# Optimization experiments

Hardware: AMD Instinct MI355X
Metric: run time of the kernel (lower is better)

## Reference

```python
import jax, jax.numpy as jnp
import numpy as np

THRESHOLD = 0.05
TOP_N = 300
NMS_THR = 0.6
POST_TOP_N = 100
MIN_SIZE = 0
N_CLASS = 81
C = N_CLASS - 1
STRIDES = (8, 16, 32, 64, 128)
IMG_H, IMG_W = 800, 1024
B = 16


def _level_hw(s):
    return (-(-IMG_H // s), -(-IMG_W // s))


def setup_inputs() -> dict:
    key = jax.random.key(0)
    inp = {}
    for li, s in enumerate(STRIDES):
        H, W = _level_hw(s)
        key, k1, k2, k3 = jax.random.split(key, 4)
        xs = (jnp.arange(W, dtype=jnp.float32) + 0.5) * s
        ys = (jnp.arange(H, dtype=jnp.float32) + 0.5) * s
        gx, gy = jnp.meshgrid(xs, ys)  # [H, W], row-major h*W+w flatten order
        inp[f"location{li}"] = jnp.stack([gx.reshape(-1), gy.reshape(-1)], -1)
        inp[f"cls{li}"] = jax.random.normal(k1, (B, C, H, W), jnp.float32)
        inp[f"box{li}"] = jax.random.uniform(k2, (B, 4, H, W), jnp.float32) * (4.0 * s)
        inp[f"ctr{li}"] = jax.random.normal(k3, (B, 1, H, W), jnp.float32)
    inp["img_h"] = IMG_H
    inp["img_w"] = IMG_W
    return inp


def _process_level(loc, cls, box, ctr, img_h, img_w):
    b, c, h, w = cls.shape
    cls = jax.nn.sigmoid(cls.transpose(0, 2, 3, 1).reshape(b, h * w, c))
    box = box.transpose(0, 2, 3, 1).reshape(b, h * w, 4)
    ctr = jax.nn.sigmoid(ctr.reshape(b, h * w))
    score = cls * ctr[:, :, None]                 # [B, HW, C]
    masked = jnp.where(cls > THRESHOLD, score, -1.0).reshape(b, -1)
    k = min(TOP_N, masked.shape[1])
    vals, idx = jax.lax.top_k(masked, k)
    if k < TOP_N:
        vals = jnp.pad(vals, ((0, 0), (0, TOP_N - k)), constant_values=-1.0)
        idx = jnp.pad(idx, ((0, 0), (0, TOP_N - k)))
    valid = vals > 0.0                            # candidates only; pads invalid
    pos = idx // c
    label = idx % c + 1
    ssel = jnp.take_along_axis(score.reshape(b, -1), idx, axis=1)  # differentiable gather
    bsel = jnp.take_along_axis(box, pos[..., None], axis=1)        # [B, TOP_N, 4]
    lsel = loc[pos]                                                # [B, TOP_N, 2]
    # decode + clip (BoxList.clip clamps to [0, size-1])
    x1 = jnp.clip(lsel[..., 0] - bsel[..., 0], 0.0, img_w - 1.0)
    y1 = jnp.clip(lsel[..., 1] - bsel[..., 1], 0.0, img_h - 1.0)
    x2 = jnp.clip(lsel[..., 0] + bsel[..., 2], 0.0, img_w - 1.0)
    y2 = jnp.clip(lsel[..., 1] + bsel[..., 3], 0.0, img_h - 1.0)
    det = jnp.stack([x1, y1, x2, y2], -1)
    # remove_small_box: xywh with remove=1
    valid = valid & ((x2 - x1 + 1.0) >= MIN_SIZE) & ((y2 - y1 + 1.0) >= MIN_SIZE)
    scores = jnp.sqrt(jnp.maximum(ssel, 1e-12))
    return det, scores, label, valid


def _pairwise_iou(b):
    area = (b[:, 2] - b[:, 0]) * (b[:, 3] - b[:, 1])
    lt = jnp.maximum(b[:, None, :2], b[None, :, :2])
    rb = jnp.minimum(b[:, None, 2:], b[None, :, 2:])
    wh = jnp.clip(rb - lt, 0.0)
    inter = wh[..., 0] * wh[..., 1]
    union = area[:, None] + area[None, :] - inter
    return inter / jnp.maximum(union, 1e-9)


def _nms_image(boxes, scores, labels, valid, offset):
    # per-class NMS via class-offset trick: boxes of different labels never overlap
    K = boxes.shape[0]
    s = jnp.where(valid, scores, -jnp.inf)
    order = jnp.argsort(-s)
    b = boxes[order]
    v = valid[order]
    lab = labels[order]
    so = s[order]
    iou = _pairwise_iou(b + (lab.astype(b.dtype) * offset)[:, None])
    ar = jnp.arange(K)

    def body(i, keep):
        sup = (iou[i] > NMS_THR) & keep[i] & (ar > i)
        return keep & ~sup

    keep = jax.lax.fori_loop(0, K, body, v)
    s2 = jnp.where(keep, so, -jnp.inf)
    _, idx2 = jax.lax.top_k(s2, POST_TOP_N)   # post_top_n selection
    fvalid = jnp.take(keep, idx2)
    fb = jnp.where(fvalid[:, None], b[idx2], 0.0)
    fs = jnp.where(fvalid, so[idx2], 0.0)
    fl = jnp.where(fvalid, lab[idx2], 0)
    return fb, fs, fl, fvalid


def _forward(locs, clss, boxs, ctrs, img_h, img_w):
    dets, scs, labs, vals = [], [], [], []
    for loc, cl, bx, ct in zip(locs, clss, boxs, ctrs):
        d, s, l, v = _process_level(loc, cl, bx, ct, float(img_h), float(img_w))
        dets.append(d); scs.append(s); labs.append(l); vals.append(v)
    det = jnp.concatenate(dets, 1)   # [B, 5*TOP_N, 4]
    sc = jnp.concatenate(scs, 1)
    lab = jnp.concatenate(labs, 1)
    val = jnp.concatenate(vals, 1)
    offset = float(max(img_h, img_w) + 1)
    fb, fs, fl, fv = jax.vmap(lambda b_, s_, l_, v_: _nms_image(b_, s_, l_, v_, offset))(det, sc, lab, val)
    out5 = jnp.concatenate([fb, fs[..., None]], -1)  # [B, POST_TOP_N, 5]
    return out5, fl, fv


def reference(location0, location1, location2, location3, location4,
              cls0, cls1, cls2, cls3, cls4,
              box0, box1, box2, box3, box4,
              ctr0, ctr1, ctr2, ctr3, ctr4,
              img_h, img_w):
    locs = [location0, location1, location2, location3, location4]
    clss = [cls0, cls1, cls2, cls3, cls4]
    boxs = [box0, box1, box2, box3, box4]
    ctrs = [ctr0, ctr1, ctr2, ctr3, ctr4]
    return _forward(locs, clss, boxs, ctrs, img_h, img_w)
```

## Files before the change

### kernel.cpp

```cpp
#include <hip/hip_runtime.h>
#include <math.h>

#define THREADS 256
#define SORTT 1024

constexpr int NLEV  = 5;
constexpr int NB    = 16;
constexpr int NC    = 80;
constexpr int TOPN  = 300;
constexpr int KC    = NLEV * TOPN;
constexpr int KROWS = 1536;
constexpr int WORDS = 24;
constexpr int POSTN = 100;
constexpr int CAP   = 4096;
constexpr int NBINS = 2048;
constexpr int NPAIR = NLEV * NB;

constexpr int HW0 = 12800, HW1 = 3200, HW2 = 800, HW3 = 208, HW4 = 56;
constexpr int CH0 = 63, CH1 = 16, CH2 = 4, CH3 = 2, CH4 = 1;
constexpr int CHUNKS = CH0 + CH1 + CH2 + CH3 + CH4;
constexpr int CHUNK_ELEMS = 16384;

constexpr int SCTB0 = 0;
constexpr int SCTB1 = 204800;
constexpr int SCTB2 = 256000;
constexpr int SCTB3 = 268800;
constexpr int SCTB4 = 272128;
constexpr int SCTN  = 273024;

constexpr int GPL0 = 4000, GPL1 = 1000, GPL2 = 250, GPL3 = 65, GPL4 = 18;
constexpr int GMXB0 = 0;
constexpr int GMXB1 = GMXB0 + NB * GPL0;
constexpr int GMXB2 = GMXB1 + NB * GPL1;
constexpr int GMXB3 = GMXB2 + NB * GPL2;
constexpr int GMXB4 = GMXB3 + NB * GPL3;
constexpr int GMXN  = GMXB4 + NB * GPL4;

constexpr size_t align256(size_t x) { return (x + 255) & ~(size_t)255; }
constexpr size_t OFF_HIST = 0;
constexpr size_t OFF_CNT  = OFF_HIST + (size_t)NPAIR * NBINS * 4;
constexpr size_t OFF_CAND = align256(OFF_CNT + (size_t)NPAIR * 4);
constexpr size_t OFF_CBOX = align256(OFF_CAND + (size_t)NPAIR * CAP * 8);
constexpr size_t OFF_CSC  = align256(OFF_CBOX + (size_t)NB * KC * 4 * 4);
constexpr size_t OFF_CLB  = align256(OFF_CSC  + (size_t)NB * KC * 4);
constexpr size_t OFF_SSC  = align256(OFF_CLB  + (size_t)NB * KC * 4);
constexpr size_t OFF_SLB  = align256(OFF_SSC  + (size_t)NB * KC * 4);
constexpr size_t OFF_SBOX = align256(OFF_SLB  + (size_t)NB * KC * 4);
constexpr size_t OFF_OBOX = align256(OFF_SBOX + (size_t)NB * KC * 4 * 4);
constexpr size_t OFF_M    = align256(OFF_OBOX + (size_t)NB * KC * 4 * 4);
constexpr size_t OFF_SCT  = align256(OFF_M + (size_t)NB * KROWS * WORDS * 8);
constexpr size_t OFF_GMX  = align256(OFF_SCT + (size_t)SCTN * 4);
constexpr size_t OFF_TV   = align256(OFF_GMX + (size_t)GMXN * 2);

struct Cand { float s; int i; };

__device__ __forceinline__ float sigm(float x) { return 1.0f / (1.0f + expf(-x)); }

__device__ __forceinline__ float sigf(float x) {
#if __has_builtin(__builtin_amdgcn_exp2f) && __has_builtin(__builtin_amdgcn_rcpf)
    float e = __builtin_amdgcn_exp2f(__fmul_rn(x, -1.44269504088896340736f));
    return __builtin_amdgcn_rcpf(__fadd_rn(1.0f, e));
#else
    return 1.0f / (1.0f + __expf(-x));
#endif
}

__device__ __forceinline__ unsigned scoreKey(float s) {
    unsigned b = __float_as_uint(s);
    unsigned k = (b < 0x3E800000u) ? 0u : ((b - 0x3E800000u) >> 13);
    return (k > 2047u) ? 2047u : k;
}

__device__ __forceinline__ unsigned long long readlane64(unsigned long long v, int l) {
    unsigned lo = (unsigned)__builtin_amdgcn_readlane((int)(unsigned)(v & 0xffffffffull), l);
    unsigned hi = (unsigned)__builtin_amdgcn_readlane((int)(unsigned)(v >> 32), l);
    return ((unsigned long long)hi << 32) | lo;
}

__device__ void bitonicShared(float* ss, int* si, int N) {
    for (int k = 2; k <= N; k <<= 1) {
        for (int j = k >> 1; j > 0; j >>= 1) {
            __syncthreads();
            for (int i = threadIdx.x; i < N; i += blockDim.x) {
                int ixj = i ^ j;
                if (ixj > i) {
                    float s1 = ss[i], s2 = ss[ixj];
                    int a1 = si[i], a2 = si[ixj];
                    bool bef = (s1 > s2) || (s1 == s2 && a1 < a2);
                    bool up = ((i & k) == 0);
                    if (up ? !bef : bef) { ss[i] = s2; ss[ixj] = s1; si[i] = a2; si[ixj] = a1; }
                }
            }
        }
    }
    __syncthreads();
}

__global__ __launch_bounds__(THREADS) void k_init(
        const float* t0, const float* t1, const float* t2, const float* t3, const float* t4,
        float* __restrict__ sct, unsigned* __restrict__ zp, int zn) {
    int i = blockIdx.x * THREADS + threadIdx.x;
    if (i < zn) zp[i] = 0;
    if (i < SCTN) {
        float x;
        if (i < SCTB1)      x = t0[i - SCTB0];
        else if (i < SCTB2) x = t1[i - SCTB1];
        else if (i < SCTB3) x = t2[i - SCTB2];
        else if (i < SCTB4) x = t3[i - SCTB3];
        else                x = t4[i - SCTB4];
        sct[i] = sigm(x);
    }
}

template<int HW, int SCTB, int GPL, int GMXB>
__device__ __forceinline__ void histChunkV(int chunkLocal, int b,
        const float* __restrict__ cls, const float* __restrict__ sct,
        unsigned short* __restrict__ gmx, unsigned* __restrict__ h) {
    constexpr int NE = HW * NC;
    const float* cp = cls + (size_t)b * NE;
    const float* tb = sct + SCTB + b * HW;
    unsigned short* gp = gmx + GMXB + (size_t)b * GPL;
    int w = threadIdx.x >> 6, lane = threadIdx.x & 63;
    int half = lane >> 5, hlane = lane & 31;
    for (int bi = w; bi < 32; bi += 4) {
        int ebase = (chunkLocal * 32 + bi) * 512;
        if (ebase >= NE) break;
        int e = ebase + lane * 8;
        int kmax = 0;
        if (e < NE) {
            int c = e / HW; int hwb = e - c * HW;
            float4 xa = *(const float4*)(cp + e);
            float4 xb = *(const float4*)(cp + e + 4);
            float4 ta = *(const float4*)(tb + hwb);
            float4 tc = *(const float4*)(tb + hwb + 4);
            float xs[8] = {xa.x, xa.y, xa.z, xa.w, xb.x, xb.y, xb.z, xb.w};
            float ts[8] = {ta.x, ta.y, ta.z, ta.w, tc.x, tc.y, tc.z, tc.w};
            #pragma unroll
            for (int q = 0; q < 8; ++q) {
                float scls = sigf(xs[q]);
                float s = __fmul_rn(scls, ts[q]);
                unsigned key = scoreKey(s);
                if (key) atomicAdd(&h[key], 1u);
                kmax = max(kmax, (int)key);
            }
        }
        #pragma unroll
        for (int sh = 1; sh < 32; sh <<= 1) kmax = max(kmax, __shfl_xor(kmax, sh, 64));
        int g = (ebase >> 8) + half;
        if (hlane == 0 && g * 256 < NE) gp[g] = (unsigned short)kmax;
    }
}

__global__ __launch_bounds__(THREADS) void k_hist(
        const float* c0, const float* c1, const float* c2, const float* c3, const float* c4,
        const float* __restrict__ sct, unsigned short* __restrict__ gmx, unsigned* ghist) {
    __shared__ unsigned h[NBINS];
    for (int k = threadIdx.x; k < NBINS; k += THREADS) h[k] = 0;
    __syncthreads();
    int cx = blockIdx.x, b = blockIdx.y;
    int li;
    if (cx < CH0)                 { histChunkV<HW0,SCTB0,GPL0,GMXB0>(cx, b, c0, sct, gmx, h); li = 0; }
    else if (cx < CH0+CH1)        { histChunkV<HW1,SCTB1,GPL1,GMXB1>(cx-CH0, b, c1, sct, gmx, h); li = 1; }
    else if (cx < CH0+CH1+CH2)    { histChunkV<HW2,SCTB2,GPL2,GMXB2>(cx-CH0-CH1, b, c2, sct, gmx, h); li = 2; }
    else if (cx < CH0+CH1+CH2+CH3){ histChunkV<HW3,SCTB3,GPL3,GMXB3>(cx-CH0-CH1-CH2, b, c3, sct, gmx, h); li = 3; }
    else                          { histChunkV<HW4,SCTB4,GPL4,GMXB4>(cx-CH0-CH1-CH2-CH3, b, c4, sct, gmx, h); li = 4; }
    __syncthreads();
    unsigned* gp = ghist + (size_t)(li * NB + b) * NBINS;
    for (int k = threadIdx.x; k < NBINS; k += THREADS) {
        unsigned v = h[k];
        if (v) atomicAdd(&gp[k], v);
    }
}

__global__ __launch_bounds__(THREADS) void k_thresh(
        const unsigned* __restrict__ ghist, unsigned* __restrict__ tvs) {
    __shared__ unsigned seg[THREADS];
    int pid = blockIdx.x;
    const unsigned* h = ghist + (size_t)pid * NBINS;
    constexpr int SB = NBINS / THREADS;
    unsigned s = 0;
    for (int k = 0; k < SB; ++k) s += h[threadIdx.x * SB + k];
    seg[threadIdx.x] = s;
    __syncthreads();
    if (threadIdx.x == 0) {
        unsigned acc = 0; unsigned TA = 0;
        int t = THREADS - 1;
        for (; t >= 0; --t) {
            if (acc + seg[t] >= (unsigned)TOPN) break;
            acc += seg[t];
        }
        if (t >= 0) {
            int lo = t * SB;
            int bin = lo + SB - 1;
            for (; bin >= lo; --bin) { acc += h[bin]; if (acc >= (unsigned)TOPN) break; }
            TA = (unsigned)max(bin, lo);
        }
        tvs[pid] = (TA >= 1) ? (TA - 1) : 0;
    }
}

constexpr int LBUF = 1024;
constexpr int GB = 8;

template<int HW, int SCTB, int GPL, int GMXB>
__device__ __forceinline__ void collectChunkV(int chunkLocal, int b, int li, unsigned Tv,
        const float* __restrict__ cls, const float* __restrict__ sct,
        const unsigned short* __restrict__ gmx,
        Cand* __restrict__ candAll, unsigned* __restrict__ cnt,
        Cand* __restrict__ lbuf, unsigned* __restrict__ lcnt,
        short* __restrict__ glist, int* __restrict__ gcnt) {
    constexpr int NE = HW * NC;
    int pid = li * NB + b;
    Cand* cd = candAll + (size_t)pid * CAP;
    const float* cp = cls + (size_t)b * NE;
    const float* tb = sct + SCTB + b * HW;
    const unsigned short* gp = gmx + GMXB + (size_t)b * GPL;
    if (threadIdx.x < 64) {
        int g = chunkLocal * 64 + threadIdx.x;
        bool ok = ((size_t)g * 256 < (size_t)NE);
        if (ok && Tv) ok = ((unsigned)gp[g] + 1u >= Tv);
        unsigned long long m = __ballot(ok);
        int pos = __popcll(m & ((1ull << threadIdx.x) - 1ull));
        if (ok) glist[pos] = (short)g;
        if (threadIdx.x == 0) *gcnt = __popcll(m);
    }
    __syncthreads();
    int n = *gcnt;
    for (int base = 0; base < n; base += GB) {
        float xv[GB], tv[GB];
        int ev[GB];
        bool okv[GB];
        #pragma unroll
        for (int q = 0; q < GB; ++q) {
            int gi = base + q;
            int g = glist[(gi < n) ? gi : 0];
            int e = g * 256 + (int)threadIdx.x;
            bool ok = (gi < n) && (e < NE);
            e = ok ? e : 0;
            int c = e / HW; int hw = e - c * HW;
            xv[q] = cp[e];
            tv[q] = tb[hw];
            ev[q] = e;
            okv[q] = ok;
        }
        __builtin_amdgcn_sched_barrier(0);
        #pragma unroll
        for (int q = 0; q < GB; ++q) {
            float scls = sigm(xv[q]);
            float s = __fmul_rn(scls, tv[q]);
            unsigned key = scoreKey(s);
            bool take = okv[q] && (Tv ? (key >= Tv) : (scls > 0.05f));
            if (take) {
                int e = ev[q];
                int c = e / HW; int hw = e - c * HW;
                unsigned slot = atomicAdd(lcnt, 1u);
                if (slot < (unsigned)LBUF) { lbuf[slot].s = s; lbuf[slot].i = hw * NC + c; }
                else {
                    unsigned gs = atomicAdd(&cnt[pid], 1u);
                    if (gs < (unsigned)CAP) { cd[gs].s = s; cd[gs].i = hw * NC + c; }
                }
            }
        }
    }
}

__global__ __launch_bounds__(THREADS) void k_collect(
        const float* c0, const float* c1, const float* c2, const float* c3, const float* c4,
        const float* __restrict__ sct, const unsigned short* __restrict__ gmx,
        const unsigned* __restrict__ tvs, Cand* cand, unsigned* cnt) {
    __shared__ Cand lbuf[LBUF];
    __shared__ unsigned lcnt, gbase;
    __shared__ short glist[64];
    __shared__ int gcnt;
    if (threadIdx.x == 0) lcnt = 0;
    int cx = blockIdx.x, b = blockIdx.y;
    int li, cl;
    if (cx < CH0)                  { li = 0; cl = cx; }
    else if (cx < CH0+CH1)         { li = 1; cl = cx - CH0; }
    else if (cx < CH0+CH1+CH2)     { li = 2; cl = cx - CH0 - CH1; }
    else if (cx < CH0+CH1+CH2+CH3) { li = 3; cl = cx - CH0 - CH1 - CH2; }
    else                           { li = 4; cl = cx - CH0 - CH1 - CH2 - CH3; }
    int pid = li * NB + b;
    unsigned Tv = tvs[pid];
    switch (li) {
        case 0: collectChunkV<HW0,SCTB0,GPL0,GMXB0>(cl, b, 0, Tv, c0, sct, gmx, cand, cnt, lbuf, &lcnt, glist, &gcnt); break;
        case 1: collectChunkV<HW1,SCTB1,GPL1,GMXB1>(cl, b, 1, Tv, c1, sct, gmx, cand, cnt, lbuf, &lcnt, glist, &gcnt); break;
        case 2: collectChunkV<HW2,SCTB2,GPL2,GMXB2>(cl, b, 2, Tv, c2, sct, gmx, cand, cnt, lbuf, &lcnt, glist, &gcnt); break;
        case 3: collectChunkV<HW3,SCTB3,GPL3,GMXB3>(cl, b, 3, Tv, c3, sct, gmx, cand, cnt, lbuf, &lcnt, glist, &gcnt); break;
        default: collectChunkV<HW4,SCTB4,GPL4,GMXB4>(cl, b, 4, Tv, c4, sct, gmx, cand, cnt, lbuf, &lcnt, glist, &gcnt); break;
    }
    __syncthreads();
    unsigned n = lcnt; if (n > (unsigned)LBUF) n = LBUF;
    if (threadIdx.x == 0) gbase = n ? atomicAdd(&cnt[pid], n) : 0u;
    __syncthreads();
    Cand* cd = cand + (size_t)pid * CAP;
    for (unsigned i = threadIdx.x; i < n; i += THREADS) {
        unsigned s = gbase + i;
        if (s < (unsigned)CAP) cd[s] = lbuf[i];
    }
}

__global__ __launch_bounds__(THREADS) void k_select(
        const Cand* __restrict__ candAll, const unsigned* __restrict__ cntAll,
        const float* l0, const float* l1, const float* l2, const float* l3, const float* l4,
        const float* b0, const float* b1, const float* b2, const float* b3, const float* b4,
        float* __restrict__ cbox, float* __restrict__ csc, int* __restrict__ clb) {
    __shared__ float ss[CAP];
    __shared__ int si[CAP];
    int pid = blockIdx.x;
    int li = pid / NB, b = pid - li * NB;
    int n = (int)min(cntAll[pid], (unsigned)CAP);
    const Cand* cd = candAll + (size_t)pid * CAP;
    int N = 2; while (N < n) N <<= 1;
    for (int k = threadIdx.x; k < N; k += THREADS) {
        if (k < n) { ss[k] = cd[k].s; si[k] = cd[k].i; }
        else       { ss[k] = -INFINITY; si[k] = 0x40000000 + k; }
    }
    __syncthreads();
    bitonicShared(ss, si, N);

    const float* locp; const float* boxp; int HW;
    switch (li) {
        case 0: locp = l0; boxp = b0; HW = HW0; break;
        case 1: locp = l1; boxp = b1; HW = HW1; break;
        case 2: locp = l2; boxp = b2; HW = HW2; break;
        case 3: locp = l3; boxp = b3; HW = HW3; break;
        default: locp = l4; boxp = b4; HW = HW4; break;
    }
    for (int j = threadIdx.x; j < TOPN; j += THREADS) {
        int cidx = b * KC + li * TOPN + j;
        bool ok = (j < n);
        float s = ok ? ss[j] : -INFINITY;
        ok = ok && (s > 0.0f);
        if (ok) {
            int idx = si[j];
            int hw = idx / NC, c = idx - hw * NC;
            float lx = locp[hw * 2 + 0], ly = locp[hw * 2 + 1];
            const float* bp = boxp + (size_t)b * 4 * HW + hw;
            float bl = bp[0], bt = bp[HW], br = bp[2 * HW], bb = bp[3 * HW];
            float x1 = fminf(fmaxf(__fsub_rn(lx, bl), 0.0f), 1023.0f);
            float y1 = fminf(fmaxf(__fsub_rn(ly, bt), 0.0f),  799.0f);
            float x2 = fminf(fmaxf(__fadd_rn(lx, br), 0.0f), 1023.0f);
            float y2 = fminf(fmaxf(__fadd_rn(ly, bb), 0.0f),  799.0f);
            cbox[cidx * 4 + 0] = x1; cbox[cidx * 4 + 1] = y1;
            cbox[cidx * 4 + 2] = x2; cbox[cidx * 4 + 3] = y2;
            csc[cidx] = sqrtf(fmaxf(s, 1e-12f));
            clb[cidx] = c + 1;
        } else {
            cbox[cidx * 4 + 0] = 0.0f; cbox[cidx * 4 + 1] = 0.0f;
            cbox[cidx * 4 + 2] = 0.0f; cbox[cidx * 4 + 3] = 0.0f;
            csc[cidx] = -INFINITY;
            clb[cidx] = 0;
        }
    }
}

__global__ __launch_bounds__(SORTT) void k_sortimg(
        const float* __restrict__ csc, const int* __restrict__ clb, const float* __restrict__ cbox,
        float* __restrict__ ssc, int* __restrict__ slb, float* __restrict__ sbox, float* __restrict__ obox) {
    int b = blockIdx.x;
    __shared__ float ss[2048];
    __shared__ int si[2048];
    for (int k = threadIdx.x; k < 2048; k += SORTT) {
        if (k < KC) { ss[k] = csc[b * KC + k]; si[k] = k; }
        else        { ss[k] = -INFINITY; si[k] = 0x40000000 + k; }
    }
    __syncthreads();
    bitonicShared(ss, si, 2048);
    for (int k = threadIdx.x; k < KC; k += SORTT) {
        int sl = si[k];
        int src = b * KC + sl;
        int dst = b * KC + k;
        float sc = ss[k];
        int lab = clb[src];
        ssc[dst] = sc; slb[dst] = lab;
        float off = __fmul_rn((float)lab, 1025.0f);
        #pragma unroll
        for (int q = 0; q < 4; ++q) {
            float v = cbox[src * 4 + q];
            sbox[dst * 4 + q] = v;
            obox[dst * 4 + q] = __fadd_rn(v, off);
        }
    }
}

__global__ __launch_bounds__(64) void k_iou(const float* __restrict__ obox,
                                            unsigned long long* __restrict__ MT) {
    int w = blockIdx.x, tile = blockIdx.y, b = blockIdx.z;
    if (w < tile) return;
    int lane = threadIdx.x;
    __shared__ float4 sj[64];
    __shared__ float aj[64];
    const float4* op = (const float4*)obox + (size_t)b * KC;
    int j0 = w * 64;
    int jl = j0 + lane;
    float4 vj = op[(jl < KC) ? jl : (KC - 1)];
    sj[lane] = vj;
    aj[lane] = __fmul_rn(__fsub_rn(vj.z, vj.x), __fsub_rn(vj.w, vj.y));
    int i = tile * 64 + lane;
    float4 bi = op[(i < KC) ? i : (KC - 1)];
    float ai = __fmul_rn(__fsub_rn(bi.z, bi.x), __fsub_rn(bi.w, bi.y));
    __syncthreads();
    unsigned long long bits = 0;
    int jmax = min(64, KC - j0);
    for (int jj = 0; jj < jmax; ++jj) {
        float4 bj = sj[jj];
        float xx1 = fmaxf(bi.x, bj.x), yy1 = fmaxf(bi.y, bj.y);
        float xx2 = fminf(bi.z, bj.z), yy2 = fminf(bi.w, bj.w);
        float ww = fmaxf(__fsub_rn(xx2, xx1), 0.0f);
        float hh = fmaxf(__fsub_rn(yy2, yy1), 0.0f);
        float inter = __fmul_rn(ww, hh);
        float uni = __fsub_rn(__fadd_rn(ai, aj[jj]), inter);
        float iou = __fdiv_rn(inter, fmaxf(uni, 1e-9f));
        bool kp = ((j0 + jj) > i) && (iou > 0.6f);
        bits |= kp ? (1ull << jj) : 0ull;
    }
    if (i >= KC) bits = 0;
    MT[((size_t)b * WORDS + w) * KROWS + i] = bits;
}

__global__ __launch_bounds__(64) void k_nms(
        const unsigned long long* __restrict__ MT, const float* __restrict__ ssc,
        const int* __restrict__ slb, const float* __restrict__ sbox, float* __restrict__ out) {
    int b = blockIdx.x, lane = threadIdx.x;
    for (int k = lane; k < POSTN * 5; k += 64) out[(size_t)b * POSTN * 5 + k] = 0.0f;
    for (int k = lane; k < POSTN; k += 64) {
        out[(size_t)NB * POSTN * 5 + b * POSTN + k] = 0.0f;
        out[(size_t)NB * POSTN * 5 + NB * POSTN + b * POSTN + k] = 0.0f;
    }
    const float* sp = ssc + b * KC;
    unsigned long long validV = 0;
    for (int c = 0; c < WORDS; ++c) {
        int i = c * 64 + lane;
        bool f = (i < KC) && (sp[i] > 0.0f);
        unsigned long long m = __ballot(f);
        validV = (lane == c) ? m : validV;
    }
    unsigned long long mybit = 1ull << lane;
    unsigned long long keptV = 0;
    const unsigned long long* Mb = MT + (size_t)b * WORDS * KROWS;

    unsigned long long pv[WORDS];
    pv[0] = Mb[lane];

    int keptTotal = 0;
    for (int t = 0; t < WORDS; ++t) {
        int tn = (t + 1 < WORDS) ? (t + 1) : t;
        const unsigned long long* cp = Mb + (size_t)tn * KROWS + lane;
        unsigned long long nv[WORDS];
        #pragma unroll
        for (int c = 0; c < WORDS; ++c) {
            int cc = (c <= tn) ? c : 0;
            nv[c] = cp[(size_t)cc * 64];
        }
        __builtin_amdgcn_sched_barrier(0);

        unsigned long long D = pv[t];
        unsigned long long acc = 0;
        #pragma unroll
        for (int c = 0; c < WORDS; ++c) {
            if (c < t) {
                unsigned long long kc = readlane64(keptV, c);
                if (kc & mybit) acc |= pv[c];
            }
        }
        #pragma unroll
        for (int s = 1; s < 64; s <<= 1) acc |= __shfl_xor(acc, s, 64);

        unsigned long long validT = readlane64(validV, t);
        unsigned long long rem = acc;
        unsigned long long sup = __ballot(D != 0ull) & validT;
        unsigned long long todoS = sup;
        while (todoS) {
            int r = __builtin_ctzll(todoS);
            todoS &= todoS - 1;
            if (!((rem >> r) & 1ull)) {
                unsigned long long Dr = readlane64(D, r);
                rem |= Dr;
                todoS &= ~Dr;
            }
        }
        unsigned long long kept = validT & ~rem;
        keptV = (lane == t) ? kept : keptV;

        keptTotal += (int)__popcll(kept);
        if (keptTotal >= POSTN) break;

        #pragma unroll
        for (int c = 0; c < WORDS; ++c) pv[c] = nv[c];
    }

    int base = 0;
    for (int c = 0; c < WORDS && base < POSTN; ++c) {
        unsigned long long kw = readlane64(keptV, c);
        bool f = (kw & mybit) != 0ull;
        int rank = base + __popcll(kw & (mybit - 1ull));
        if (f && rank < POSTN) {
            int i = c * 64 + lane;
            int src = b * KC + i;
            float* o5 = out + ((size_t)b * POSTN + rank) * 5;
            o5[0] = sbox[src * 4 + 0]; o5[1] = sbox[src * 4 + 1];
            o5[2] = sbox[src * 4 + 2]; o5[3] = sbox[src * 4 + 3];
            o5[4] = ssc[src];
            out[(size_t)NB * POSTN * 5 + b * POSTN + rank] = (float)slb[src];
            out[(size_t)NB * POSTN * 5 + NB * POSTN + b * POSTN + rank] = 1.0f;
        }
        base += __popcll(kw);
    }
}

extern "C" void kernel_launch(void* const* d_in, const int* in_sizes, int n_in,
                              void* d_out, int out_size, void* d_ws, size_t ws_size,
                              hipStream_t stream) {
    const float *loc[5], *cls[5], *box[5], *ctr[5];
    for (int l = 0; l < 5; ++l) {
        loc[l] = (const float*)d_in[l * 4 + 0];
        cls[l] = (const float*)d_in[l * 4 + 1];
        box[l] = (const float*)d_in[l * 4 + 2];
        ctr[l] = (const float*)d_in[l * 4 + 3];
    }
    char* ws = (char*)d_ws;
    unsigned* hist = (unsigned*)(ws + OFF_HIST);
    unsigned* cnt  = (unsigned*)(ws + OFF_CNT);
    Cand* cand     = (Cand*)(ws + OFF_CAND);
    float* cbox    = (float*)(ws + OFF_CBOX);
    float* csc     = (float*)(ws + OFF_CSC);
    int*   clb     = (int*)(ws + OFF_CLB);
    float* ssc     = (float*)(ws + OFF_SSC);
    int*   slb     = (int*)(ws + OFF_SLB);
    float* sbox    = (float*)(ws + OFF_SBOX);
    float* obox    = (float*)(ws + OFF_OBOX);
    unsigned long long* MT = (unsigned long long*)(ws + OFF_M);
    float* sct     = (float*)(ws + OFF_SCT);
    unsigned short* gmx = (unsigned short*)(ws + OFF_GMX);
    unsigned* tvs  = (unsigned*)(ws + OFF_TV);
    float* out = (float*)d_out;

    int zn = (int)(OFF_CAND / 4);
    int initBlocks = (max(zn, SCTN) + THREADS - 1) / THREADS;
    k_init<<<initBlocks, THREADS, 0, stream>>>(
        ctr[0], ctr[1], ctr[2], ctr[3], ctr[4], sct, (unsigned*)ws, zn);
    k_hist<<<dim3(CHUNKS, NB), THREADS, 0, stream>>>(
        cls[0], cls[1], cls[2], cls[3], cls[4], sct, gmx, hist);
    k_thresh<<<NPAIR, THREADS, 0, stream>>>(hist, tvs);
    k_collect<<<dim3(CHUNKS, NB), THREADS, 0, stream>>>(
        cls[0], cls[1], cls[2], cls[3], cls[4], sct, gmx, tvs, cand, cnt);
    k_select<<<NPAIR, THREADS, 0, stream>>>(
        cand, cnt,
        loc[0], loc[1], loc[2], loc[3], loc[4],
        box[0], box[1], box[2], box[3], box[4],
        cbox, csc, clb);
    k_sortimg<<<NB, SORTT, 0, stream>>>(csc, clb, cbox, ssc, slb, sbox, obox);
    k_iou<<<dim3(WORDS, WORDS, NB), 64, 0, stream>>>(obox, MT);
    k_nms<<<NB, 64, 0, stream>>>(MT, ssc, slb, sbox, out);
}
```

Baseline: 290.6 us.

## Compact surviving groups globally and replace bitonic sorts with rank sorts

The threshold kernel now scans the per-group max table and appends every group that can pass the threshold to one global work list. A grid-stride collect kernel then processes only those listed groups, using wave-aggregated atomics instead of a shared-memory staging buffer. The bitonic sorts in select and in the per-image sort are replaced by O(n^2) rank counting: each element counts how many precede it and scatters directly to its rank. This removes many barrier-separated passes, at the cost of quadratic comparisons when candidate counts are large.

```diff
diff --git a/kernel.cpp b/kernel.cpp
--- a/kernel.cpp
+++ b/kernel.cpp
@@ -19,7 +19,6 @@
 constexpr int HW0 = 12800, HW1 = 3200, HW2 = 800, HW3 = 208, HW4 = 56;
 constexpr int CH0 = 63, CH1 = 16, CH2 = 4, CH3 = 2, CH4 = 1;
 constexpr int CHUNKS = CH0 + CH1 + CH2 + CH3 + CH4;
-constexpr int CHUNK_ELEMS = 16384;
 
 constexpr int SCTB0 = 0;
 constexpr int SCTB1 = 204800;
@@ -35,6 +34,8 @@
 constexpr int GMXB3 = GMXB2 + NB * GPL2;
 constexpr int GMXB4 = GMXB3 + NB * GPL3;
 constexpr int GMXN  = GMXB4 + NB * GPL4;
+
+constexpr int GLCAP = 96 * 1024;
 
 constexpr size_t align256(size_t x) { return (x + 255) & ~(size_t)255; }
 constexpr size_t OFF_HIST = 0;
@@ -51,6 +52,8 @@
 constexpr size_t OFF_SCT  = align256(OFF_M + (size_t)NB * KROWS * WORDS * 8);
 constexpr size_t OFF_GMX  = align256(OFF_SCT + (size_t)SCTN * 4);
 constexpr size_t OFF_TV   = align256(OFF_GMX + (size_t)GMXN * 2);
+constexpr size_t OFF_GCNT = align256(OFF_TV + (size_t)NPAIR * 4);
+constexpr size_t OFF_GL   = align256(OFF_GCNT + 256);
 
 struct Cand { float s; int i; };
 
@@ -77,29 +80,15 @@
     return ((unsigned long long)hi << 32) | lo;
 }
 
-__device__ void bitonicShared(float* ss, int* si, int N) {
-    for (int k = 2; k <= N; k <<= 1) {
-        for (int j = k >> 1; j > 0; j >>= 1) {
-            __syncthreads();
-            for (int i = threadIdx.x; i < N; i += blockDim.x) {
-                int ixj = i ^ j;
-                if (ixj > i) {
-                    float s1 = ss[i], s2 = ss[ixj];
-                    int a1 = si[i], a2 = si[ixj];
-                    bool bef = (s1 > s2) || (s1 == s2 && a1 < a2);
-                    bool up = ((i & k) == 0);
-                    if (up ? !bef : bef) { ss[i] = s2; ss[ixj] = s1; si[i] = a2; si[ixj] = a1; }
-                }
-            }
-        }
-    }
-    __syncthreads();
+__device__ __forceinline__ int cmpBefore(float sj, int ij, float sk, int ik) {
+    return (sj > sk) || (sj == sk && ij < ik);
 }
 
 __global__ __launch_bounds__(THREADS) void k_init(
         const float* t0, const float* t1, const float* t2, const float* t3, const float* t4,
-        float* __restrict__ sct, unsigned* __restrict__ zp, int zn) {
+        float* __restrict__ sct, unsigned* __restrict__ zp, int zn, unsigned* __restrict__ gcount) {
     int i = blockIdx.x * THREADS + threadIdx.x;
+    if (i == 0) *gcount = 0;
     if (i < zn) zp[i] = 0;
     if (i < SCTN) {
         float x;
@@ -173,9 +162,12 @@
 }
 
 __global__ __launch_bounds__(THREADS) void k_thresh(
-        const unsigned* __restrict__ ghist, unsigned* __restrict__ tvs) {
+        const unsigned* __restrict__ ghist, const unsigned short* __restrict__ gmx,
+        unsigned* __restrict__ tvs, unsigned* __restrict__ gcount, unsigned* __restrict__ glist) {
     __shared__ unsigned seg[THREADS];
+    __shared__ unsigned shTv;
     int pid = blockIdx.x;
+    int li = pid >> 4, b = pid & 15;
     const unsigned* h = ghist + (size_t)pid * NBINS;
     constexpr int SB = NBINS / THREADS;
     unsigned s = 0;
@@ -195,108 +187,90 @@
             for (; bin >= lo; --bin) { acc += h[bin]; if (acc >= (unsigned)TOPN) break; }
             TA = (unsigned)max(bin, lo);
         }
-        tvs[pid] = (TA >= 1) ? (TA - 1) : 0;
-    }
-}
-
-constexpr int LBUF = 1024;
-constexpr int GB = 8;
-
-template<int HW, int SCTB, int GPL, int GMXB>
-__device__ __forceinline__ void collectChunkV(int chunkLocal, int b, int li, unsigned Tv,
+        unsigned Tv = (TA >= 1) ? (TA - 1) : 0;
+        shTv = Tv;
+        tvs[pid] = Tv;
+    }
+    __syncthreads();
+    unsigned Tv = shTv;
+    int GPL, GMXB;
+    switch (li) {
+        case 0: GPL = GPL0; GMXB = GMXB0; break;
+        case 1: GPL = GPL1; GMXB = GMXB1; break;
+        case 2: GPL = GPL2; GMXB = GMXB2; break;
+        case 3: GPL = GPL3; GMXB = GMXB3; break;
+        default: GPL = GPL4; GMXB = GMXB4; break;
+    }
+    const unsigned short* gp = gmx + GMXB + (size_t)b * GPL;
+    for (int g0 = 0; g0 < GPL; g0 += THREADS) {
+        int g = g0 + (int)threadIdx.x;
+        bool ok = (g < GPL);
+        if (ok && Tv) ok = ((unsigned)gp[g] + 1u >= Tv);
+        unsigned long long m = __ballot(ok);
+        int nW = __popcll(m);
+        if (nW) {
+            unsigned base = 0;
+            if ((threadIdx.x & 63) == 0) base = atomicAdd(gcount, (unsigned)nW);
+            base = (unsigned)__builtin_amdgcn_readfirstlane((int)base);
+            if (ok) {
+                unsigned slot = base + (unsigned)__popcll(m & ((1ull << (threadIdx.x & 63)) - 1ull));
+                if (slot < (unsigned)GLCAP) glist[slot] = ((unsigned)pid << 12) | (unsigned)g;
+            }
+        }
+    }
+}
+
+template<int HW, int SCTB>
+__device__ __forceinline__ void procGroup(int g, int b, int pid, unsigned Tv,
         const float* __restrict__ cls, const float* __restrict__ sct,
-        const unsigned short* __restrict__ gmx,
-        Cand* __restrict__ candAll, unsigned* __restrict__ cnt,
-        Cand* __restrict__ lbuf, unsigned* __restrict__ lcnt,
-        short* __restrict__ glist, int* __restrict__ gcnt) {
+        Cand* __restrict__ cd, unsigned* __restrict__ cnt) {
     constexpr int NE = HW * NC;
-    int pid = li * NB + b;
-    Cand* cd = candAll + (size_t)pid * CAP;
     const float* cp = cls + (size_t)b * NE;
     const float* tb = sct + SCTB + b * HW;
-    const unsigned short* gp = gmx + GMXB + (size_t)b * GPL;
-    if (threadIdx.x < 64) {
-        int g = chunkLocal * 64 + threadIdx.x;
-        bool ok = ((size_t)g * 256 < (size_t)NE);
-        if (ok && Tv) ok = ((unsigned)gp[g] + 1u >= Tv);
-        unsigned long long m = __ballot(ok);
-        int pos = __popcll(m & ((1ull << threadIdx.x) - 1ull));
-        if (ok) glist[pos] = (short)g;
-        if (threadIdx.x == 0) *gcnt = __popcll(m);
-    }
-    __syncthreads();
-    int n = *gcnt;
-    for (int base = 0; base < n; base += GB) {
-        float xv[GB], tv[GB];
-        int ev[GB];
-        bool okv[GB];
-        #pragma unroll
-        for (int q = 0; q < GB; ++q) {
-            int gi = base + q;
-            int g = glist[(gi < n) ? gi : 0];
-            int e = g * 256 + (int)threadIdx.x;
-            bool ok = (gi < n) && (e < NE);
-            e = ok ? e : 0;
-            int c = e / HW; int hw = e - c * HW;
-            xv[q] = cp[e];
-            tv[q] = tb[hw];
-            ev[q] = e;
-            okv[q] = ok;
-        }
-        __builtin_amdgcn_sched_barrier(0);
-        #pragma unroll
-        for (int q = 0; q < GB; ++q) {
-            float scls = sigm(xv[q]);
-            float s = __fmul_rn(scls, tv[q]);
-            unsigned key = scoreKey(s);
-            bool take = okv[q] && (Tv ? (key >= Tv) : (scls > 0.05f));
-            if (take) {
-                int e = ev[q];
-                int c = e / HW; int hw = e - c * HW;
-                unsigned slot = atomicAdd(lcnt, 1u);
-                if (slot < (unsigned)LBUF) { lbuf[slot].s = s; lbuf[slot].i = hw * NC + c; }
-                else {
-                    unsigned gs = atomicAdd(&cnt[pid], 1u);
-                    if (gs < (unsigned)CAP) { cd[gs].s = s; cd[gs].i = hw * NC + c; }
-                }
-            }
+    int e = g * 256 + (int)threadIdx.x;
+    bool ok = (e < NE);
+    int ee = ok ? e : 0;
+    int c = ee / HW; int hw = ee - c * HW;
+    float x = cp[ee];
+    float t = tb[hw];
+    float scls = sigm(x);
+    float s = __fmul_rn(scls, t);
+    unsigned key = scoreKey(s);
+    bool take = ok && (Tv ? (key >= Tv) : (scls > 0.05f));
+    unsigned long long m = __ballot(take);
+    int nW = __popcll(m);
+    if (nW) {
+        unsigned base = 0;
+        if ((threadIdx.x & 63) == 0) base = atomicAdd(&cnt[pid], (unsigned)nW);
+        base = (unsigned)__builtin_amdgcn_readfirstlane((int)base);
+        if (take) {
+            unsigned slot = base + (unsigned)__popcll(m & ((1ull << (threadIdx.x & 63)) - 1ull));
+            if (slot < (unsigned)CAP) { cd[slot].s = s; cd[slot].i = hw * NC + c; }
         }
     }
 }
 
 __global__ __launch_bounds__(THREADS) void k_collect(
         const float* c0, const float* c1, const float* c2, const float* c3, const float* c4,
-        const float* __restrict__ sct, const unsigned short* __restrict__ gmx,
-        const unsigned* __restrict__ tvs, Cand* cand, unsigned* cnt) {
-    __shared__ Cand lbuf[LBUF];
-    __shared__ unsigned lcnt, gbase;
-    __shared__ short glist[64];
-    __shared__ int gcnt;
-    if (threadIdx.x == 0) lcnt = 0;
-    int cx = blockIdx.x, b = blockIdx.y;
-    int li, cl;
-    if (cx < CH0)                  { li = 0; cl = cx; }
-    else if (cx < CH0+CH1)         { li = 1; cl = cx - CH0; }
-    else if (cx < CH0+CH1+CH2)     { li = 2; cl = cx - CH0 - CH1; }
-    else if (cx < CH0+CH1+CH2+CH3) { li = 3; cl = cx - CH0 - CH1 - CH2; }
-    else                           { li = 4; cl = cx - CH0 - CH1 - CH2 - CH3; }
-    int pid = li * NB + b;
-    unsigned Tv = tvs[pid];
-    switch (li) {
-        case 0: collectChunkV<HW0,SCTB0,GPL0,GMXB0>(cl, b, 0, Tv, c0, sct, gmx, cand, cnt, lbuf, &lcnt, glist, &gcnt); break;
-        case 1: collectChunkV<HW1,SCTB1,GPL1,GMXB1>(cl, b, 1, Tv, c1, sct, gmx, cand, cnt, lbuf, &lcnt, glist, &gcnt); break;
-        case 2: collectChunkV<HW2,SCTB2,GPL2,GMXB2>(cl, b, 2, Tv, c2, sct, gmx, cand, cnt, lbuf, &lcnt, glist, &gcnt); break;
-        case 3: collectChunkV<HW3,SCTB3,GPL3,GMXB3>(cl, b, 3, Tv, c3, sct, gmx, cand, cnt, lbuf, &lcnt, glist, &gcnt); break;
-        default: collectChunkV<HW4,SCTB4,GPL4,GMXB4>(cl, b, 4, Tv, c4, sct, gmx, cand, cnt, lbuf, &lcnt, glist, &gcnt); break;
-    }
-    __syncthreads();
-    unsigned n = lcnt; if (n > (unsigned)LBUF) n = LBUF;
-    if (threadIdx.x == 0) gbase = n ? atomicAdd(&cnt[pid], n) : 0u;
-    __syncthreads();
-    Cand* cd = cand + (size_t)pid * CAP;
-    for (unsigned i = threadIdx.x; i < n; i += THREADS) {
-        unsigned s = gbase + i;
-        if (s < (unsigned)CAP) cd[s] = lbuf[i];
+        const float* __restrict__ sct, const unsigned* __restrict__ tvs,
+        const unsigned* __restrict__ gcount, const unsigned* __restrict__ glist,
+        Cand* cand, unsigned* cnt) {
+    unsigned n = *gcount;
+    if (n > (unsigned)GLCAP) n = GLCAP;
+    for (unsigned gi = blockIdx.x; gi < n; gi += gridDim.x) {
+        unsigned entry = glist[gi];
+        int pid = (int)(entry >> 12);
+        int g = (int)(entry & 4095u);
+        int li = pid >> 4, b = pid & 15;
+        unsigned Tv = tvs[pid];
+        Cand* cd = cand + (size_t)pid * CAP;
+        switch (li) {
+            case 0: procGroup<HW0,SCTB0>(g, b, pid, Tv, c0, sct, cd, cnt); break;
+            case 1: procGroup<HW1,SCTB1>(g, b, pid, Tv, c1, sct, cd, cnt); break;
+            case 2: procGroup<HW2,SCTB2>(g, b, pid, Tv, c2, sct, cd, cnt); break;
+            case 3: procGroup<HW3,SCTB3>(g, b, pid, Tv, c3, sct, cd, cnt); break;
+            default: procGroup<HW4,SCTB4>(g, b, pid, Tv, c4, sct, cd, cnt); break;
+        }
     }
 }
 
@@ -305,19 +279,18 @@
         const float* l0, const float* l1, const float* l2, const float* l3, const float* l4,
         const float* b0, const float* b1, const float* b2, const float* b3, const float* b4,
         float* __restrict__ cbox, float* __restrict__ csc, int* __restrict__ clb) {
-    __shared__ float ss[CAP];
-    __shared__ int si[CAP];
+    __shared__ __align__(16) float ss[CAP + 4];
+    __shared__ __align__(16) int si[CAP + 4];
     int pid = blockIdx.x;
-    int li = pid / NB, b = pid - li * NB;
+    int li = pid >> 4, b = pid & 15;
     int n = (int)min(cntAll[pid], (unsigned)CAP);
+    int npad = (n + 3) & ~3;
     const Cand* cd = candAll + (size_t)pid * CAP;
-    int N = 2; while (N < n) N <<= 1;
-    for (int k = threadIdx.x; k < N; k += THREADS) {
+    for (int k = threadIdx.x; k < npad; k += THREADS) {
         if (k < n) { ss[k] = cd[k].s; si[k] = cd[k].i; }
-        else       { ss[k] = -INFINITY; si[k] = 0x40000000 + k; }
-    }
-    __syncthreads();
-    bitonicShared(ss, si, N);
+        else       { ss[k] = -INFINITY; si[k] = 0x7fffffff; }
+    }
+    __syncthreads();
 
     const float* locp; const float* boxp; int HW;
     switch (li) {
@@ -327,30 +300,56 @@
         case 3: locp = l3; boxp = b3; HW = HW3; break;
         default: locp = l4; boxp = b4; HW = HW4; break;
     }
-    for (int j = threadIdx.x; j < TOPN; j += THREADS) {
+
+    for (int j = n + (int)threadIdx.x; j < TOPN; j += THREADS) {
         int cidx = b * KC + li * TOPN + j;
-        bool ok = (j < n);
-        float s = ok ? ss[j] : -INFINITY;
-        ok = ok && (s > 0.0f);
-        if (ok) {
-            int idx = si[j];
-            int hw = idx / NC, c = idx - hw * NC;
-            float lx = locp[hw * 2 + 0], ly = locp[hw * 2 + 1];
-            const float* bp = boxp + (size_t)b * 4 * HW + hw;
-            float bl = bp[0], bt = bp[HW], br = bp[2 * HW], bb = bp[3 * HW];
-            float x1 = fminf(fmaxf(__fsub_rn(lx, bl), 0.0f), 1023.0f);
-            float y1 = fminf(fmaxf(__fsub_rn(ly, bt), 0.0f),  799.0f);
-            float x2 = fminf(fmaxf(__fadd_rn(lx, br), 0.0f), 1023.0f);
-            float y2 = fminf(fmaxf(__fadd_rn(ly, bb), 0.0f),  799.0f);
-            cbox[cidx * 4 + 0] = x1; cbox[cidx * 4 + 1] = y1;
-            cbox[cidx * 4 + 2] = x2; cbox[cidx * 4 + 3] = y2;
-            csc[cidx] = sqrtf(fmaxf(s, 1e-12f));
-            clb[cidx] = c + 1;
-        } else {
-            cbox[cidx * 4 + 0] = 0.0f; cbox[cidx * 4 + 1] = 0.0f;
-            cbox[cidx * 4 + 2] = 0.0f; cbox[cidx * 4 + 3] = 0.0f;
-            csc[cidx] = -INFINITY;
-            clb[cidx] = 0;
+        cbox[cidx * 4 + 0] = 0.0f; cbox[cidx * 4 + 1] = 0.0f;
+        cbox[cidx * 4 + 2] = 0.0f; cbox[cidx * 4 + 3] = 0.0f;
+        csc[cidx] = -INFINITY;
+        clb[cidx] = 0;
+    }
+
+    for (int k0 = 0; k0 < n; k0 += THREADS * 4) {
+        int kA = k0 + (int)threadIdx.x;
+        int kB = kA + THREADS, kC2 = kA + 2 * THREADS, kD = kA + 3 * THREADS;
+        float sA = (kA < n) ? ss[kA] : 0.0f; int iA = (kA < n) ? si[kA] : 0;
+        float sB = (kB < n) ? ss[kB] : 0.0f; int iB = (kB < n) ? si[kB] : 0;
+        float sC = (kC2 < n) ? ss[kC2] : 0.0f; int iC = (kC2 < n) ? si[kC2] : 0;
+        float sD = (kD < n) ? ss[kD] : 0.0f; int iD = (kD < n) ? si[kD] : 0;
+        int rA = 0, rB = 0, rC = 0, rD = 0;
+        for (int j = 0; j < npad; j += 4) {
+            float4 v = *(const float4*)&ss[j];
+            int4 w = *(const int4*)&si[j];
+            rA += cmpBefore(v.x, w.x, sA, iA) + cmpBefore(v.y, w.y, sA, iA)
+                + cmpBefore(v.z, w.z, sA, iA) + cmpBefore(v.w, w.w, sA, iA);
+            rB += cmpBefore(v.x, w.x, sB, iB) + cmpBefore(v.y, w.y, sB, iB)
+                + cmpBefore(v.z, w.z, sB, iB) + cmpBefore(v.w, w.w, sB, iB);
+            rC += cmpBefore(v.x, w.x, sC, iC) + cmpBefore(v.y, w.y, sC, iC)
+                + cmpBefore(v.z, w.z, sC, iC) + cmpBefore(v.w, w.w, sC, iC);
+            rD += cmpBefore(v.x, w.x, sD, iD) + cmpBefore(v.y, w.y, sD, iD)
+                + cmpBefore(v.z, w.z, sD, iD) + cmpBefore(v.w, w.w, sD, iD);
+        }
+        #pragma unroll
+        for (int q = 0; q < 4; ++q) {
+            int k = kA + q * THREADS;
+            int r = (q == 0) ? rA : (q == 1) ? rB : (q == 2) ? rC : rD;
+            float s = (q == 0) ? sA : (q == 1) ? sB : (q == 2) ? sC : sD;
+            int idx = (q == 0) ? iA : (q == 1) ? iB : (q == 2) ? iC : iD;
+            if (k < n && r < TOPN) {
+                int cidx = b * KC + li * TOPN + r;
+                int hw = idx / NC, c = idx - hw * NC;
+                float lx = locp[hw * 2 + 0], ly = locp[hw * 2 + 1];
+                const float* bp = boxp + (size_t)b * 4 * HW + hw;
+                float bl = bp[0], bt = bp[HW], br = bp[2 * HW], bb = bp[3 * HW];
+                float x1 = fminf(fmaxf(__fsub_rn(lx, bl), 0.0f), 1023.0f);
+                float y1 = fminf(fmaxf(__fsub_rn(ly, bt), 0.0f),  799.0f);
+                float x2 = fminf(fmaxf(__fadd_rn(lx, br), 0.0f), 1023.0f);
+                float y2 = fminf(fmaxf(__fadd_rn(ly, bb), 0.0f),  799.0f);
+                cbox[cidx * 4 + 0] = x1; cbox[cidx * 4 + 1] = y1;
+                cbox[cidx * 4 + 2] = x2; cbox[cidx * 4 + 3] = y2;
+                csc[cidx] = sqrtf(fmaxf(s, 1e-12f));
+                clb[cidx] = c + 1;
+            }
         }
     }
 }
@@ -359,27 +358,42 @@
         const float* __restrict__ csc, const int* __restrict__ clb, const float* __restrict__ cbox,
         float* __restrict__ ssc, int* __restrict__ slb, float* __restrict__ sbox, float* __restrict__ obox) {
     int b = blockIdx.x;
-    __shared__ float ss[2048];
-    __shared__ int si[2048];
-    for (int k = threadIdx.x; k < 2048; k += SORTT) {
-        if (k < KC) { ss[k] = csc[b * KC + k]; si[k] = k; }
-        else        { ss[k] = -INFINITY; si[k] = 0x40000000 + k; }
-    }
-    __syncthreads();
-    bitonicShared(ss, si, 2048);
-    for (int k = threadIdx.x; k < KC; k += SORTT) {
-        int sl = si[k];
-        int src = b * KC + sl;
-        int dst = b * KC + k;
-        float sc = ss[k];
-        int lab = clb[src];
-        ssc[dst] = sc; slb[dst] = lab;
-        float off = __fmul_rn((float)lab, 1025.0f);
-        #pragma unroll
-        for (int q = 0; q < 4; ++q) {
-            float v = cbox[src * 4 + q];
-            sbox[dst * 4 + q] = v;
-            obox[dst * 4 + q] = __fadd_rn(v, off);
+    __shared__ __align__(16) float ss[1504];
+    for (int k = threadIdx.x; k < 1504; k += SORTT)
+        ss[k] = (k < KC) ? csc[b * KC + k] : -INFINITY;
+    __syncthreads();
+    int k1 = (int)threadIdx.x;
+    int k2 = k1 + SORTT;
+    float s1 = ss[k1];
+    float s2 = (k2 < KC) ? ss[k2] : 0.0f;
+    int r1 = 0, r2 = 0;
+    for (int j = 0; j < 1504; j += 4) {
+        float4 v = *(const float4*)&ss[j];
+        r1 += ((v.x > s1) || (v.x == s1 && (j + 0) < k1))
+            + ((v.y > s1) || (v.y == s1 && (j + 1) < k1))
+            + ((v.z > s1) || (v.z == s1 && (j + 2) < k1))
+            + ((v.w > s1) || (v.w == s1 && (j + 3) < k1));
+        r2 += ((v.x > s2) || (v.x == s2 && (j + 0) < k2))
+            + ((v.y > s2) || (v.y == s2 && (j + 1) < k2))
+            + ((v.z > s2) || (v.z == s2 && (j + 2) < k2))
+            + ((v.w > s2) || (v.w == s2 && (j + 3) < k2));
+    }
+    #pragma unroll
+    for (int q = 0; q < 2; ++q) {
+        int k = (q == 0) ? k1 : k2;
+        int r = (q == 0) ? r1 : r2;
+        if (k < KC) {
+            int src = b * KC + k, dst = b * KC + r;
+            float sc = ss[k];
+            int lab = clb[src];
+            ssc[dst] = sc; slb[dst] = lab;
+            float off = __fmul_rn((float)lab, 1025.0f);
+            float4 v = *(const float4*)&cbox[(size_t)src * 4];
+            *(float4*)&sbox[(size_t)dst * 4] = v;
+            float4 o;
+            o.x = __fadd_rn(v.x, off); o.y = __fadd_rn(v.y, off);
+            o.z = __fadd_rn(v.z, off); o.w = __fadd_rn(v.w, off);
+            *(float4*)&obox[(size_t)dst * 4] = o;
         }
     }
 }
@@ -534,17 +548,19 @@
     float* sct     = (float*)(ws + OFF_SCT);
     unsigned short* gmx = (unsigned short*)(ws + OFF_GMX);
     unsigned* tvs  = (unsigned*)(ws + OFF_TV);
+    unsigned* gcount = (unsigned*)(ws + OFF_GCNT);
+    unsigned* glist  = (unsigned*)(ws + OFF_GL);
     float* out = (float*)d_out;
 
     int zn = (int)(OFF_CAND / 4);
     int initBlocks = (max(zn, SCTN) + THREADS - 1) / THREADS;
     k_init<<<initBlocks, THREADS, 0, stream>>>(
-        ctr[0], ctr[1], ctr[2], ctr[3], ctr[4], sct, (unsigned*)ws, zn);
+        ctr[0], ctr[1], ctr[2], ctr[3], ctr[4], sct, (unsigned*)ws, zn, gcount);
     k_hist<<<dim3(CHUNKS, NB), THREADS, 0, stream>>>(
         cls[0], cls[1], cls[2], cls[3], cls[4], sct, gmx, hist);
-    k_thresh<<<NPAIR, THREADS, 0, stream>>>(hist, tvs);
-    k_collect<<<dim3(CHUNKS, NB), THREADS, 0, stream>>>(
-        cls[0], cls[1], cls[2], cls[3], cls[4], sct, gmx, tvs, cand, cnt);
+    k_thresh<<<NPAIR, THREADS, 0, stream>>>(hist, gmx, tvs, gcount, glist);
+    k_collect<<<4096, THREADS, 0, stream>>>(
+        cls[0], cls[1], cls[2], cls[3], cls[4], sct, tvs, gcount, glist, cand, cnt);
     k_select<<<NPAIR, THREADS, 0, stream>>>(
         cand, cnt,
         loc[0], loc[1], loc[2], loc[3], loc[4],
```

Result: slower. 455.3 us (+56.7%).
